# Kernel optimization log

Measured on AMD Instinct MI355X. Metric: run time of the kernel, lower is better.

Reference implementation:

```python
import jax, jax.numpy as jnp
import numpy as np

N = 100000   # nodes
E = 1600000  # edges
F_IN = 128
H = 128
C = 40


def setup_inputs() -> dict:
    key = jax.random.key(0)
    ks = jax.random.split(key, 8)
    s = 0.05
    return {
        "x": jax.random.normal(ks[0], (N, F_IN), dtype=jnp.float32),
        "edge_index": jax.random.randint(ks[1], (2, E), 0, N, dtype=jnp.int32),
        "W1": jax.random.normal(ks[2], (F_IN, H), dtype=jnp.float32) * s,
        "b1": jnp.zeros((H,), jnp.float32),
        "W2": jax.random.normal(ks[3], (H, H), dtype=jnp.float32) * s,
        "b2": jnp.zeros((H,), jnp.float32),
        "Wfc": jax.random.normal(ks[4], (H, C), dtype=jnp.float32) * s,
        "bfc": jnp.zeros((C,), jnp.float32),
    }


def _graph_conv(x, src, dst, norm_out, norm_in, W, b):
    # DGL GraphConv, norm='both': h = D_in^{-1/2} A D_out^{-1/2} x W + b
    h = (x * norm_out[:, None]) @ W                      # [N, H] (W first: in>=out)
    agg = jax.ops.segment_sum(h[src], dst, num_segments=N)  # gather + scatter-add
    return agg * norm_in[:, None] + b


def reference(x, edge_index, W1, b1, W2, b2, Wfc, bfc):
    src, dst = edge_index[0], edge_index[1]
    ones = jnp.ones((E,), x.dtype)
    deg_out = jnp.maximum(jax.ops.segment_sum(ones, src, num_segments=N), 1.0)
    deg_in = jnp.maximum(jax.ops.segment_sum(ones, dst, num_segments=N), 1.0)
    norm_out = jax.lax.rsqrt(deg_out)
    norm_in = jax.lax.rsqrt(deg_in)
    # layer 0: GraphConv + relu (dropout is identity in eval mode)
    h = jax.nn.relu(_graph_conv(x, src, dst, norm_out, norm_in, W1, b1))
    # layer 1: GraphConv, no activation
    h = _graph_conv(h, src, dst, norm_out, norm_in, W2, b2)
    # final FC
    return h @ Wfc + bfc
```

## Files before the change

kernel.cpp:

```cpp
#include <hip/hip_runtime.h>
#include <hip/hip_fp16.h>


#define CHUNK    4096
#define NBK      800
#define SLAB     3072

typedef __attribute__((ext_vector_type(8))) short bf16x8;
typedef __attribute__((ext_vector_type(4))) float f32x4;

struct __align__(8)  half4 { __half x, y, z, w; };
struct __align__(16) half8 { __half h[8]; };

__device__ __forceinline__ unsigned short f2bf(float f) {
    union { float f; unsigned u; } v; v.f = f;
    unsigned r = v.u + 0x7FFFu + ((v.u >> 16) & 1u);
    return (unsigned short)(r >> 16);
}
__device__ __forceinline__ float bf2f(unsigned short h) {
    union { unsigned u; float f; } v; v.u = ((unsigned)h) << 16;
    return v.f;
}

__global__ void setup_kernel(const float* __restrict__ W1, const float* __restrict__ W2,
                             const float* __restrict__ Wfc,
                             const float* __restrict__ b2, const float* __restrict__ bfc,
                             unsigned short* __restrict__ Wh1, unsigned short* __restrict__ Wl1,
                             unsigned short* __restrict__ Wh2, unsigned short* __restrict__ Wl2,
                             float* __restrict__ b2p,
                             int* __restrict__ cur_d, int* __restrict__ cur_s, int nbuck) {
    int idx = blockIdx.x * blockDim.x + threadIdx.x;
    if (idx < nbuck) { cur_d[idx] = idx * SLAB; cur_s[idx] = idx * SLAB; }

    if (idx < 16384) {
        int k = idx >> 7, nn = idx & 127;
        float v = W1[idx];
        int q = k >> 5, j = k & 7, lb = ((k >> 3) & 3) * 16;
        int tcol = nn >> 4;
        int l = lb + (nn & 15);
        int pos = ((tcol * 4 + q) * 64 + l) * 8 + j;
        unsigned short h = f2bf(v);
        Wh1[pos] = h;
        Wl1[pos] = f2bf(v - bf2f(h));
    } else if (idx < 16384 + 6144) {
        int i2 = idx - 16384;
        int k = i2 / 48, nn = i2 - k * 48;
        float v = 0.f;
        if (nn < 40) {
            const float* w2row = W2 + k * 128;
            #pragma unroll 8
            for (int jj = 0; jj < 128; ++jj) v += w2row[jj] * Wfc[jj * 40 + nn];
        }
        int t = nn >> 4, q = k >> 5, j = k & 7;
        int l = ((k >> 3) & 3) * 16 + (nn & 15);
        int pos = ((t * 4 + q) * 64 + l) * 8 + j;
        unsigned short h = f2bf(v);
        Wh2[pos] = h;
        Wl2[pos] = f2bf(v - bf2f(h));
    } else if (idx < 16384 + 6144 + 40) {
        int c = idx - (16384 + 6144);
        float a = bfc[c];
        #pragma unroll 8
        for (int j = 0; j < 128; ++j) a += b2[j] * Wfc[j * 40 + c];
        b2p[c] = a;
    }
}

__global__ __launch_bounds__(256, 3) void fat_kernel(
        const int* __restrict__ src, const int* __restrict__ dst,
        int* __restrict__ cur_d, int* __restrict__ cur_s,
        unsigned int* __restrict__ ppack, unsigned char* __restrict__ es_loc,
        int E, int nsc,
        const float* __restrict__ X,
        const unsigned short* __restrict__ Wh, const unsigned short* __restrict__ Wl,
        __half* __restrict__ Y, int nrows) {
    __shared__ int hd[NBK], hs[NBK], bd[NBK], bs[NBK];
    const int tid = threadIdx.x;

    if (blockIdx.x < nsc) {
        for (int i = tid; i < NBK; i += 256) { hd[i] = 0; hs[i] = 0; }
        __syncthreads();
        const int base = blockIdx.x * CHUNK;
        const int end  = min(base + CHUNK, E);
        for (int e = base + tid; e < end; e += 256) {
            atomicAdd(&hd[((unsigned)dst[e]) >> 7], 1);
            atomicAdd(&hs[((unsigned)src[e]) >> 7], 1);
        }
        __syncthreads();
        for (int i = tid; i < NBK; i += 256) {
            int cd = hd[i];
            bd[i] = cd ? atomicAdd(&cur_d[i], cd) : 0;
            hd[i] = 0;
            int cs = hs[i];
            bs[i] = cs ? atomicAdd(&cur_s[i], cs) : 0;
            hs[i] = 0;
        }
        __syncthreads();
        for (int e = base + tid; e < end; e += 256) {
            int d = dst[e], s = src[e];
            unsigned bin_d = ((unsigned)d) >> 7;
            int pos = bd[bin_d] + atomicAdd(&hd[bin_d], 1);
            ppack[pos] = (((unsigned)d & 127u) << 17) | (unsigned)s;
            unsigned bin_s = ((unsigned)s) >> 7;
            int ps = bs[bin_s] + atomicAdd(&hs[bin_s], 1);
            es_loc[ps] = (unsigned char)(s & 127);
        }
        return;
    }

    const int blk  = blockIdx.x - nsc;
    const int lane = tid & 63;
    const int w    = tid >> 6;
    const int m    = lane & 15;
    const int quad = lane >> 4;
    const int rowBase = blk * 128 + w * 32;

    bf16x8 Ah[2][4], Al[2][4];
    #pragma unroll
    for (int rt = 0; rt < 2; ++rt) {
        int r = rowBase + rt * 16 + m;
        const float* xr = X + (size_t)(r < nrows ? r : 0) * 128;
        const float z = (r < nrows) ? 1.f : 0.f;
        #pragma unroll
        for (int q = 0; q < 4; ++q) {
            int k0 = q * 32 + quad * 8;
            float4 a = *(const float4*)(xr + k0);
            float4 bv = *(const float4*)(xr + k0 + 4);
            float v[8] = {a.x * z, a.y * z, a.z * z, a.w * z,
                          bv.x * z, bv.y * z, bv.z * z, bv.w * z};
            bf16x8 hi, lo;
            #pragma unroll
            for (int j = 0; j < 8; ++j) {
                unsigned short h = f2bf(v[j]);
                hi[j] = (short)h;
                lo[j] = (short)f2bf(v[j] - bf2f(h));
            }
            Ah[rt][q] = hi; Al[rt][q] = lo;
        }
    }

    f32x4 acc[2][8];
    #pragma unroll
    for (int rt = 0; rt < 2; ++rt)
        #pragma unroll
        for (int t = 0; t < 8; ++t)
            acc[rt][t] = (f32x4){0.f, 0.f, 0.f, 0.f};

    #pragma unroll
    for (int t = 0; t < 8; ++t) {
        #pragma unroll
        for (int q = 0; q < 4; ++q) {
            const int off = ((t * 4 + q) * 64 + lane) * 8;
            bf16x8 Bh = *(const bf16x8*)(Wh + off);
            bf16x8 Bl = *(const bf16x8*)(Wl + off);
            #pragma unroll
            for (int rt = 0; rt < 2; ++rt) {
                acc[rt][t] = __builtin_amdgcn_mfma_f32_16x16x32_bf16(Ah[rt][q], Bh, acc[rt][t], 0, 0, 0);
                acc[rt][t] = __builtin_amdgcn_mfma_f32_16x16x32_bf16(Ah[rt][q], Bl, acc[rt][t], 0, 0, 0);
                acc[rt][t] = __builtin_amdgcn_mfma_f32_16x16x32_bf16(Al[rt][q], Bh, acc[rt][t], 0, 0, 0);
            }
        }
    }

    #pragma unroll
    for (int rt = 0; rt < 2; ++rt) {
        int r0 = rowBase + rt * 16 + quad * 4;
        #pragma unroll
        for (int reg = 0; reg < 4; ++reg) {
            int r = r0 + reg;
            if (r >= nrows) continue;
            __half* yr = Y + (size_t)r * 128 + m;
            #pragma unroll
            for (int t = 0; t < 8; ++t)
                yr[t * 16] = __float2half(acc[rt][t][reg]);
        }
    }
}

__global__ __launch_bounds__(256) void fine_kernel(
        const unsigned int* __restrict__ ppack, const int* __restrict__ cur_d,
        const unsigned char* __restrict__ es_loc, const int* __restrict__ cur_s,
        int* __restrict__ deg_in, float* __restrict__ norm_in,
        int* __restrict__ row_ptr, int* __restrict__ csr_src,
        float* __restrict__ norm_out, int N_) {
    __shared__ int h[128];
    __shared__ int psum[128];
    const int tid = threadIdx.x;
    const int b = blockIdx.x;
    const int start = b * SLAB;
    const int node  = (b << 7) + tid;

    const int end_d = cur_d[b];
    if (tid < 128) h[tid] = 0;
    __syncthreads();
    for (int i = start + tid; i < end_d; i += 256)
        atomicAdd(&h[ppack[i] >> 17], 1);
    __syncthreads();

    int a = 0;
    if (tid < 128) { a = h[tid]; psum[tid] = a; }
    __syncthreads();
    for (int off = 1; off < 128; off <<= 1) {
        int t = 0;
        if (tid < 128 && tid >= off) t = psum[tid - off];
        __syncthreads();
        if (tid < 128) psum[tid] += t;
        __syncthreads();
    }

    if (tid < 128) {
        int base0 = psum[tid] - a + start;
        if (node < N_) {
            deg_in[node]  = a;
            row_ptr[node] = base0;
            norm_in[node] = rsqrtf((float)(a < 1 ? 1 : a));
        }
        h[tid] = base0;
    }
    __syncthreads();

    for (int i = start + tid; i < end_d; i += 256) {
        unsigned int pk = ppack[i];
        int pos = atomicAdd(&h[pk >> 17], 1);
        csr_src[pos] = (int)(pk & 0x1FFFFu);
    }
    __syncthreads();

    const int end_s = cur_s[b];
    if (tid < 128) h[tid] = 0;
    __syncthreads();
    for (int i = start + tid; i < end_s; i += 256)
        atomicAdd(&h[(int)es_loc[i]], 1);
    __syncthreads();

    if (tid < 128 && node < N_) {
        int d = h[tid];
        norm_out[node] = rsqrtf((float)(d < 1 ? 1 : d));
    }
}

__global__ __launch_bounds__(256, 4) void gather_kernel(
        const __half* __restrict__ H, const int* __restrict__ row_ptr,
        const int* __restrict__ deg, const int* __restrict__ csr_src,
        const float* __restrict__ norm_in, const float* __restrict__ b,
        const float* __restrict__ norm_out,
        const unsigned short* __restrict__ Wh2, const unsigned short* __restrict__ Wl2,
        __half* __restrict__ G, int n) {
    __shared__ unsigned short h1h[16][136];
    __shared__ unsigned short h1l[16][136];
    const int tid   = threadIdx.x;
    const int node0 = blockIdx.x * 16;
    const int g     = tid >> 4;
    const int node  = node0 + g;
    const int c     = (tid & 15) * 8;
    const bool active = node < n;

    int start = 0, cnt = 0;
    if (active) { start = row_ptr[node]; cnt = deg[node]; }
    float acc[8] = {0.f, 0.f, 0.f, 0.f, 0.f, 0.f, 0.f, 0.f};

    int j = 0;
    for (; j + 4 <= cnt; j += 4) {
        int s0 = csr_src[start + j];
        int s1 = csr_src[start + j + 1];
        int s2 = csr_src[start + j + 2];
        int s3 = csr_src[start + j + 3];
        float n0 = norm_out[s0], n1 = norm_out[s1];
        float n2 = norm_out[s2], n3 = norm_out[s3];
        half8 v0 = *(const half8*)(H + (long long)s0 * 128 + c);
        half8 v1 = *(const half8*)(H + (long long)s1 * 128 + c);
        half8 v2 = *(const half8*)(H + (long long)s2 * 128 + c);
        half8 v3 = *(const half8*)(H + (long long)s3 * 128 + c);
        #pragma unroll
        for (int k = 0; k < 8; ++k) {
            float t0 = fmaf(n0, __half2float(v0.h[k]), fmaf(n1, __half2float(v1.h[k]), acc[k]));
            acc[k] = fmaf(n2, __half2float(v2.h[k]), fmaf(n3, __half2float(v3.h[k]), t0));
        }
    }
    for (; j < cnt; ++j) {
        int s0 = csr_src[start + j];
        float n0 = norm_out[s0];
        half8 v0 = *(const half8*)(H + (long long)s0 * 128 + c);
        #pragma unroll
        for (int k = 0; k < 8; ++k) acc[k] = fmaf(n0, __half2float(v0.h[k]), acc[k]);
    }

    float ni = active ? norm_in[node]  : 0.f;
    float no = active ? norm_out[node] : 0.f;
    float4 b0  = *(const float4*)(b + c);
    float4 b1v = *(const float4*)(b + c + 4);
    float bb[8] = {b0.x, b0.y, b0.z, b0.w, b1v.x, b1v.y, b1v.z, b1v.w};
    bf16x8 hi, lo;
    #pragma unroll
    for (int k = 0; k < 8; ++k) {
        float hv = fmaxf(acc[k] * ni + bb[k], 0.f) * no;
        unsigned short h = f2bf(hv);
        hi[k] = (short)h;
        lo[k] = (short)f2bf(hv - bf2f(h));
    }
    *(bf16x8*)&h1h[g][c] = hi;
    *(bf16x8*)&h1l[g][c] = lo;
    __syncthreads();

    const int w = tid >> 6;
    if (w < 3) {
        const int lane = tid & 63;
        const int m    = lane & 15;
        const int quad = lane >> 4;

        f32x4 a3 = (f32x4){0.f, 0.f, 0.f, 0.f};
        const int t = w;
        #pragma unroll
        for (int q = 0; q < 4; ++q) {
            const int k0 = q * 32 + quad * 8;
            bf16x8 Ah = *(const bf16x8*)&h1h[m][k0];
            bf16x8 Al = *(const bf16x8*)&h1l[m][k0];
            const int off = ((t * 4 + q) * 64 + lane) * 8;
            bf16x8 Bh = *(const bf16x8*)(Wh2 + off);
            bf16x8 Bl = *(const bf16x8*)(Wl2 + off);
            a3 = __builtin_amdgcn_mfma_f32_16x16x32_bf16(Ah, Bh, a3, 0, 0, 0);
            a3 = __builtin_amdgcn_mfma_f32_16x16x32_bf16(Ah, Bl, a3, 0, 0, 0);
            a3 = __builtin_amdgcn_mfma_f32_16x16x32_bf16(Al, Bh, a3, 0, 0, 0);
        }

        const int col = t * 16 + m;
        if (col < 40) {
            const int r0 = node0 + quad * 4;
            #pragma unroll
            for (int reg = 0; reg < 4; ++reg) {
                int r = r0 + reg;
                if (r < n) G[(size_t)r * 64 + col] = __float2half(a3[reg]);
            }
        }
    }
}

__global__ __launch_bounds__(256) void gather40_kernel(
        const __half* __restrict__ G, const int* __restrict__ row_ptr,
        const int* __restrict__ deg, const int* __restrict__ csr_src,
        const float* __restrict__ norm_in, const float* __restrict__ b2p,
        float* __restrict__ out, int n) {
    const int t = blockIdx.x * 256 + threadIdx.x;
    if (t >= n * 5) return;
    const int node = t / 5;
    const int c    = (t - node * 5) * 8;

    const int start = row_ptr[node];
    const int cnt   = deg[node];
    float acc[8] = {0.f, 0.f, 0.f, 0.f, 0.f, 0.f, 0.f, 0.f};

    int j = 0;
    for (; j + 4 <= cnt; j += 4) {
        int s0 = csr_src[start + j];
        int s1 = csr_src[start + j + 1];
        int s2 = csr_src[start + j + 2];
        int s3 = csr_src[start + j + 3];
        half8 v0 = *(const half8*)(G + (long long)s0 * 64 + c);
        half8 v1 = *(const half8*)(G + (long long)s1 * 64 + c);
        half8 v2 = *(const half8*)(G + (long long)s2 * 64 + c);
        half8 v3 = *(const half8*)(G + (long long)s3 * 64 + c);
        #pragma unroll
        for (int k = 0; k < 8; ++k)
            acc[k] += (__half2float(v0.h[k]) + __half2float(v1.h[k]))
                    + (__half2float(v2.h[k]) + __half2float(v3.h[k]));
    }
    for (; j < cnt; ++j) {
        int s0 = csr_src[start + j];
        half8 v0 = *(const half8*)(G + (long long)s0 * 64 + c);
        #pragma unroll
        for (int k = 0; k < 8; ++k) acc[k] += __half2float(v0.h[k]);
    }

    float ni = norm_in[node];
    float4 o0, o1;
    o0.x = acc[0] * ni + b2p[c + 0];
    o0.y = acc[1] * ni + b2p[c + 1];
    o0.z = acc[2] * ni + b2p[c + 2];
    o0.w = acc[3] * ni + b2p[c + 3];
    o1.x = acc[4] * ni + b2p[c + 4];
    o1.y = acc[5] * ni + b2p[c + 5];
    o1.z = acc[6] * ni + b2p[c + 6];
    o1.w = acc[7] * ni + b2p[c + 7];
    float* op = out + (long long)node * 40 + c;
    *(float4*)(op)     = o0;
    *(float4*)(op + 4) = o1;
}

extern "C" void kernel_launch(void* const* d_in, const int* in_sizes, int n_in,
                              void* d_out, int out_size, void* d_ws, size_t ws_size,
                              hipStream_t stream) {
    const float* x   = (const float*)d_in[0];
    const int*   ei  = (const int*)  d_in[1];
    const float* W1  = (const float*)d_in[2];
    const float* b1  = (const float*)d_in[3];
    const float* W2  = (const float*)d_in[4];
    const float* b2  = (const float*)d_in[5];
    const float* Wfc = (const float*)d_in[6];
    const float* bfc = (const float*)d_in[7];
    float* out = (float*)d_out;

    const int N = in_sizes[0] / 128;
    const int E = in_sizes[1] / 2;
    const int* src = ei;
    const int* dst = ei + E;

    const int nbuck = (N + 127) >> 7;
    const int nsc   = (E + CHUNK - 1) / CHUNK;
    const int gemm_grid = (N + 127) / 128;

    char* p = (char*)d_ws;
    float* norm_out = (float*)p; p += (size_t)N * 4;
    float* norm_in  = (float*)p; p += (size_t)N * 4;
    float* bufA     = (float*)p; p += (size_t)N * 128 * 4;
    float* bufB     = (float*)p; p += (size_t)N * 128 * 4;
    int*   deg_in   = (int*)p;   p += (size_t)N * 4;
    int*   row_ptr  = (int*)p;   p += (size_t)N * 4;
    int*   csr_src  = (int*)p;   p += (size_t)NBK * SLAB * 4;
    int*   cur_d    = (int*)p;   p += (size_t)1024 * 4;
    int*   cur_s    = (int*)p;   p += (size_t)1024 * 4;
    float* b2p      = (float*)p; p += (size_t)64 * 4;
    unsigned short* Wh1 = (unsigned short*)p; p += (size_t)16384 * 2;
    unsigned short* Wl1 = (unsigned short*)p; p += (size_t)16384 * 2;
    unsigned short* Wh2 = (unsigned short*)p; p += (size_t)6144 * 2;
    unsigned short* Wl2 = (unsigned short*)p; p += (size_t)6144 * 2;

    unsigned int*  ppack  = (unsigned int*)bufB;
    unsigned char* es_loc = (unsigned char*)(ppack + (size_t)NBK * SLAB);

    __half* h1pre = (__half*)bufA;
    __half* G     = (__half*)bufB;

    const int T = 256;

    setup_kernel<<<(16384 + 6144 + 40 + T - 1) / T, T, 0, stream>>>(
        W1, W2, Wfc, b2, bfc, Wh1, Wl1, Wh2, Wl2, b2p, cur_d, cur_s, nbuck);
    fat_kernel<<<nsc + gemm_grid, T, 0, stream>>>(
        src, dst, cur_d, cur_s, ppack, es_loc, E, nsc,
        x, Wh1, Wl1, h1pre, N);
    fine_kernel<<<nbuck, T, 0, stream>>>(ppack, cur_d, es_loc, cur_s,
                                         deg_in, norm_in, row_ptr, csr_src,
                                         norm_out, N);
    const int gather_grid = (N + 15) / 16;
    gather_kernel<<<gather_grid, T, 0, stream>>>(h1pre, row_ptr, deg_in, csr_src,
                                                 norm_in, b1, norm_out,
                                                 Wh2, Wl2, G, N);
    gather40_kernel<<<((size_t)N * 5 + T - 1) / T, T, 0, stream>>>(
        G, row_ptr, deg_in, csr_src, norm_in, b2p, out, N);
}
```

Before: 276.6 us.

## Pair the layer-1 GEMM with the fine CSR build and split coarse scatter out

Moves the coarse bucket scatter into its own kernel with 1024-thread blocks. The layer-1 dense GEMM now shares a launch with the per-bucket fine CSR build, using even blocks for buckets and odd blocks for GEMM tiles, instead of sharing a launch with the scatter. The aim is to cut the cost of a separate fine kernel launch and to balance work differently. The trade-offs are that the scatter no longer overlaps with the GEMM, and the 1024-thread blocks may change occupancy and shared-atomic contention.

```diff
diff --git a/kernel.cpp b/kernel.cpp
--- a/kernel.cpp
+++ b/kernel.cpp
@@ -66,54 +66,117 @@
     }
 }
 
-__global__ __launch_bounds__(256, 3) void fat_kernel(
+__global__ __launch_bounds__(1024) void scatter_res_kernel(
         const int* __restrict__ src, const int* __restrict__ dst,
         int* __restrict__ cur_d, int* __restrict__ cur_s,
         unsigned int* __restrict__ ppack, unsigned char* __restrict__ es_loc,
-        int E, int nsc,
+        int E) {
+    __shared__ int hd[NBK], hs[NBK], bd[NBK], bs[NBK];
+    const int tid = threadIdx.x;
+    for (int i = tid; i < NBK; i += 1024) { hd[i] = 0; hs[i] = 0; }
+    __syncthreads();
+    const int base = blockIdx.x * CHUNK;
+    const int end  = min(base + CHUNK, E);
+    for (int e = base + tid; e < end; e += 1024) {
+        atomicAdd(&hd[((unsigned)dst[e]) >> 7], 1);
+        atomicAdd(&hs[((unsigned)src[e]) >> 7], 1);
+    }
+    __syncthreads();
+    for (int i = tid; i < NBK; i += 1024) {
+        int cd = hd[i];
+        bd[i] = cd ? atomicAdd(&cur_d[i], cd) : 0;
+        hd[i] = 0;
+        int cs = hs[i];
+        bs[i] = cs ? atomicAdd(&cur_s[i], cs) : 0;
+        hs[i] = 0;
+    }
+    __syncthreads();
+    for (int e = base + tid; e < end; e += 1024) {
+        int d = dst[e], s = src[e];
+        unsigned bin_d = ((unsigned)d) >> 7;
+        int pos = bd[bin_d] + atomicAdd(&hd[bin_d], 1);
+        ppack[pos] = (((unsigned)d & 127u) << 17) | (unsigned)s;
+        unsigned bin_s = ((unsigned)s) >> 7;
+        int ps = bs[bin_s] + atomicAdd(&hs[bin_s], 1);
+        es_loc[ps] = (unsigned char)(s & 127);
+    }
+}
+
+__global__ __launch_bounds__(256, 3) void fine_gemm_kernel(
+        const unsigned int* __restrict__ ppack, const int* __restrict__ cur_d,
+        const unsigned char* __restrict__ es_loc, const int* __restrict__ cur_s,
+        int* __restrict__ deg_in, float* __restrict__ norm_in,
+        int* __restrict__ row_ptr, int* __restrict__ csr_src,
+        float* __restrict__ norm_out, int N_,
         const float* __restrict__ X,
         const unsigned short* __restrict__ Wh, const unsigned short* __restrict__ Wl,
-        __half* __restrict__ Y, int nrows) {
-    __shared__ int hd[NBK], hs[NBK], bd[NBK], bs[NBK];
+        __half* __restrict__ Y) {
     const int tid = threadIdx.x;
 
-    if (blockIdx.x < nsc) {
-        for (int i = tid; i < NBK; i += 256) { hd[i] = 0; hs[i] = 0; }
-        __syncthreads();
-        const int base = blockIdx.x * CHUNK;
-        const int end  = min(base + CHUNK, E);
-        for (int e = base + tid; e < end; e += 256) {
-            atomicAdd(&hd[((unsigned)dst[e]) >> 7], 1);
-            atomicAdd(&hs[((unsigned)src[e]) >> 7], 1);
-        }
-        __syncthreads();
-        for (int i = tid; i < NBK; i += 256) {
-            int cd = hd[i];
-            bd[i] = cd ? atomicAdd(&cur_d[i], cd) : 0;
-            hd[i] = 0;
-            int cs = hs[i];
-            bs[i] = cs ? atomicAdd(&cur_s[i], cs) : 0;
-            hs[i] = 0;
-        }
-        __syncthreads();
-        for (int e = base + tid; e < end; e += 256) {
-            int d = dst[e], s = src[e];
-            unsigned bin_d = ((unsigned)d) >> 7;
-            int pos = bd[bin_d] + atomicAdd(&hd[bin_d], 1);
-            ppack[pos] = (((unsigned)d & 127u) << 17) | (unsigned)s;
-            unsigned bin_s = ((unsigned)s) >> 7;
-            int ps = bs[bin_s] + atomicAdd(&hs[bin_s], 1);
-            es_loc[ps] = (unsigned char)(s & 127);
+    if ((blockIdx.x & 1) == 0) {
+        __shared__ int h[128];
+        __shared__ int psum[128];
+        const int b = blockIdx.x >> 1;
+        const int start = b * SLAB;
+        const int node  = (b << 7) + tid;
+
+        const int end_d = cur_d[b];
+        if (tid < 128) h[tid] = 0;
+        __syncthreads();
+        for (int i = start + tid; i < end_d; i += 256)
+            atomicAdd(&h[ppack[i] >> 17], 1);
+        __syncthreads();
+
+        int a = 0;
+        if (tid < 128) { a = h[tid]; psum[tid] = a; }
+        __syncthreads();
+        for (int off = 1; off < 128; off <<= 1) {
+            int t = 0;
+            if (tid < 128 && tid >= off) t = psum[tid - off];
+            __syncthreads();
+            if (tid < 128) psum[tid] += t;
+            __syncthreads();
+        }
+
+        if (tid < 128) {
+            int base0 = psum[tid] - a + start;
+            if (node < N_) {
+                deg_in[node]  = a;
+                row_ptr[node] = base0;
+                norm_in[node] = rsqrtf((float)(a < 1 ? 1 : a));
+            }
+            h[tid] = base0;
+        }
+        __syncthreads();
+
+        for (int i = start + tid; i < end_d; i += 256) {
+            unsigned int pk = ppack[i];
+            int pos = atomicAdd(&h[pk >> 17], 1);
+            csr_src[pos] = (int)(pk & 0x1FFFFu);
+        }
+        __syncthreads();
+
+        const int end_s = cur_s[b];
+        if (tid < 128) h[tid] = 0;
+        __syncthreads();
+        for (int i = start + tid; i < end_s; i += 256)
+            atomicAdd(&h[(int)es_loc[i]], 1);
+        __syncthreads();
+
+        if (tid < 128 && node < N_) {
+            int d = h[tid];
+            norm_out[node] = rsqrtf((float)(d < 1 ? 1 : d));
         }
         return;
     }
 
-    const int blk  = blockIdx.x - nsc;
+    const int blk  = blockIdx.x >> 1;
     const int lane = tid & 63;
     const int w    = tid >> 6;
     const int m    = lane & 15;
     const int quad = lane >> 4;
     const int rowBase = blk * 128 + w * 32;
+    const int nrows = N_;
 
     bf16x8 Ah[2][4], Al[2][4];
     #pragma unroll
@@ -174,68 +237,6 @@
             for (int t = 0; t < 8; ++t)
                 yr[t * 16] = __float2half(acc[rt][t][reg]);
         }
-    }
-}
-
-__global__ __launch_bounds__(256) void fine_kernel(
-        const unsigned int* __restrict__ ppack, const int* __restrict__ cur_d,
-        const unsigned char* __restrict__ es_loc, const int* __restrict__ cur_s,
-        int* __restrict__ deg_in, float* __restrict__ norm_in,
-        int* __restrict__ row_ptr, int* __restrict__ csr_src,
-        float* __restrict__ norm_out, int N_) {
-    __shared__ int h[128];
-    __shared__ int psum[128];
-    const int tid = threadIdx.x;
-    const int b = blockIdx.x;
-    const int start = b * SLAB;
-    const int node  = (b << 7) + tid;
-
-    const int end_d = cur_d[b];
-    if (tid < 128) h[tid] = 0;
-    __syncthreads();
-    for (int i = start + tid; i < end_d; i += 256)
-        atomicAdd(&h[ppack[i] >> 17], 1);
-    __syncthreads();
-
-    int a = 0;
-    if (tid < 128) { a = h[tid]; psum[tid] = a; }
-    __syncthreads();
-    for (int off = 1; off < 128; off <<= 1) {
-        int t = 0;
-        if (tid < 128 && tid >= off) t = psum[tid - off];
-        __syncthreads();
-        if (tid < 128) psum[tid] += t;
-        __syncthreads();
-    }
-
-    if (tid < 128) {
-        int base0 = psum[tid] - a + start;
-        if (node < N_) {
-            deg_in[node]  = a;
-            row_ptr[node] = base0;
-            norm_in[node] = rsqrtf((float)(a < 1 ? 1 : a));
-        }
-        h[tid] = base0;
-    }
-    __syncthreads();
-
-    for (int i = start + tid; i < end_d; i += 256) {
-        unsigned int pk = ppack[i];
-        int pos = atomicAdd(&h[pk >> 17], 1);
-        csr_src[pos] = (int)(pk & 0x1FFFFu);
-    }
-    __syncthreads();
-
-    const int end_s = cur_s[b];
-    if (tid < 128) h[tid] = 0;
-    __syncthreads();
-    for (int i = start + tid; i < end_s; i += 256)
-        atomicAdd(&h[(int)es_loc[i]], 1);
-    __syncthreads();
-
-    if (tid < 128 && node < N_) {
-        int d = h[tid];
-        norm_out[node] = rsqrtf((float)(d < 1 ? 1 : d));
     }
 }
 
@@ -405,8 +406,7 @@
     const int* dst = ei + E;
 
     const int nbuck = (N + 127) >> 7;
-    const int nsc   = (E + CHUNK - 1) / CHUNK;
-    const int gemm_grid = (N + 127) / 128;
+    const int B1 = (E + CHUNK - 1) / CHUNK;
 
     char* p = (char*)d_ws;
     float* norm_out = (float*)p; p += (size_t)N * 4;
@@ -434,12 +434,11 @@
 
     setup_kernel<<<(16384 + 6144 + 40 + T - 1) / T, T, 0, stream>>>(
         W1, W2, Wfc, b2, bfc, Wh1, Wl1, Wh2, Wl2, b2p, cur_d, cur_s, nbuck);
-    fat_kernel<<<nsc + gemm_grid, T, 0, stream>>>(
-        src, dst, cur_d, cur_s, ppack, es_loc, E, nsc,
-        x, Wh1, Wl1, h1pre, N);
-    fine_kernel<<<nbuck, T, 0, stream>>>(ppack, cur_d, es_loc, cur_s,
-                                         deg_in, norm_in, row_ptr, csr_src,
-                                         norm_out, N);
+    scatter_res_kernel<<<B1, 1024, 0, stream>>>(src, dst, cur_d, cur_s,
+                                                ppack, es_loc, E);
+    fine_gemm_kernel<<<2 * nbuck, T, 0, stream>>>(
+        ppack, cur_d, es_loc, cur_s, deg_in, norm_in, row_ptr, csr_src,
+        norm_out, N, x, Wh1, Wl1, h1pre);
     const int gather_grid = (N + 15) / 16;
     gather_kernel<<<gather_grid, T, 0, stream>>>(h1pre, row_ptr, deg_in, csr_src,
                                                  norm_in, b1, norm_out,
```

Measured after the change: 271.0 us. -2.0%, faster.
